# Optimization experiments

Hardware: AMD Instinct MI355X
Metric: run time of the kernel (lower is better)

The kernel has to match this reference:

```python
import jax, jax.numpy as jnp
import numpy as np

BN_EPS = 1e-5
L2_EPS = 1e-12  # F.normalize eps
K = 9           # kernel_size (dilation=1 so effective k = 9)
GROUPS = 4      # hard-coded groups in MRConv2d


def setup_inputs() -> dict:
    key = jax.random.key(0)
    k1, k2, k3 = jax.random.split(key, 3)
    B, C, H, W = 32, 192, 28, 28
    Cout = 384
    x = jax.random.normal(k1, (B, C, H, W), jnp.float32)
    # Conv2d(2C, Cout, 1, groups=4) weight is [Cout, 2C//4, 1, 1]; store as [Cout, 2C//4]
    fan_in = 2 * C // GROUPS
    conv_w = jax.random.normal(k2, (Cout, fan_in), jnp.float32) * np.sqrt(2.0 / fan_in)
    conv_b = jax.random.normal(k3, (Cout,), jnp.float32) * 0.05
    gamma = jnp.ones((Cout,), jnp.float32)
    beta = jnp.zeros((Cout,), jnp.float32)
    return {"x": x, "conv_w": conv_w, "conv_b": conv_b, "gamma": gamma, "beta": beta}


def _knn_idx(xf, k):
    """xf: (B, C, N) -> nn_idx: (B, N, k) via L2-normalized pairwise distance + topk."""
    xn = xf / jnp.maximum(jnp.linalg.norm(xf, axis=1, keepdims=True), L2_EPS)
    xt = xn.transpose(0, 2, 1)                       # (B, N, C)
    sq = jnp.sum(xt * xt, axis=-1, keepdims=True)    # (B, N, 1)
    inner = jnp.einsum('bnc,bmc->bnm', xt, xt)       # (B, N, N)
    dist = sq - 2.0 * inner + sq.transpose(0, 2, 1)
    _, nn_idx = jax.lax.top_k(-dist, k)              # (B, N, k)
    return nn_idx


def _forward(x, conv_w, conv_b, gamma, beta):
    B, C, H, W = x.shape
    N = H * W
    xf = x.reshape(B, C, N)
    # KNN graph built on detached features (torch: no_grad + x.detach for y when r=1)
    y = jax.lax.stop_gradient(xf)
    nn_idx = _knn_idx(y, K)                                            # (B, N, K)
    # gather neighbor features: xj[b,c,n,kk] = y[b,c,nn_idx[b,n,kk]]
    xj = jax.vmap(lambda yb, ib: yb[:, ib])(y, nn_idx)                 # (B, C, N, K)
    # max-relative: max_k (x_j - x_i); center gather of edge_index[1] is just xf
    rel = jnp.max(xj - xf[:, :, :, None], axis=-1)                     # (B, C, N)
    # cat([x.unsqueeze(2), rel.unsqueeze(2)], dim=2).reshape(B, 2C, N): channel-interleaved
    h = jnp.stack([xf, rel], axis=2).reshape(B, 2 * C, N)
    # grouped 1x1 conv, groups=4
    Cin = 2 * C
    Cout = conv_w.shape[0]
    hg = h.reshape(B, GROUPS, Cin // GROUPS, N)
    wg = conv_w.reshape(GROUPS, Cout // GROUPS, Cin // GROUPS)
    out = jnp.einsum('bgin,goi->bgon', hg, wg).reshape(B, Cout, N)
    out = out + conv_b[None, :, None]
    # BatchNorm2d (training-mode batch stats, biased variance)
    mean = jnp.mean(out, axis=(0, 2), keepdims=True)
    var = jnp.var(out, axis=(0, 2), keepdims=True)
    out = (out - mean) * jax.lax.rsqrt(var + BN_EPS)
    out = out * gamma[None, :, None] + beta[None, :, None]
    # exact (erf-based) GELU, matching torch.nn.GELU default
    out = jax.nn.gelu(out, approximate=False)
    return out.reshape(B, Cout, H, W)


def reference(x, conv_w, conv_b, gamma, beta):
    return _forward(x, conv_w, conv_b, gamma, beta)
```

## Files before the change

kernel.cpp:

```cpp
#include <hip/hip_runtime.h>

#define B_    32
#define C_    192
#define N_    784
#define NP_   1024
#define K_    9
#define COUT_ 384
#define NPTS_ (B_ * N_)
#define NTILES_ 224
#define DKW_  836

typedef __attribute__((ext_vector_type(8))) short short8;
typedef __attribute__((ext_vector_type(4))) float f32x4;

__device__ __forceinline__ unsigned int ford(float f) {
  unsigned int u = __float_as_uint(f);
  return u ^ ((u & 0x80000000u) ? 0xFFFFFFFFu : 0x80000000u);
}
__device__ __forceinline__ unsigned short f2bf(float f) {
  unsigned int u = __float_as_uint(f);
  u += 0x7FFFu + ((u >> 16) & 1u);
  return (unsigned short)(u >> 16);
}
__device__ __forceinline__ float bf2f(unsigned short h) {
  return __uint_as_float(((unsigned int)h) << 16);
}

__global__ __launch_bounds__(256) void norm_kernel(
    const float* __restrict__ x, short8* __restrict__ fragH,
    short8* __restrict__ fragL, float* __restrict__ sqp) {
  int t = threadIdx.x;
  int pl = t & 63, cg = t >> 6;
  int p = blockIdx.x * 64 + pl;
  int b = p / N_, n = p % N_;
  const float* xb = x + (size_t)b * C_ * N_ + n;

  __shared__ float red[4][64];
  __shared__ float nrmS[64];

  float part = 0.f;
  #pragma unroll 8
  for (int j = 0; j < 48; j++) {
    float v = xb[(size_t)(cg * 48 + j) * N_];
    part = __fmaf_rn(v, v, part);
  }
  red[cg][pl] = part;
  __syncthreads();
  if (t < 64) {
    float ssq = __fadd_rn(__fadd_rn(red[0][t], red[1][t]),
                          __fadd_rn(red[2][t], red[3][t]));
    nrmS[t] = fmaxf(__fsqrt_rn(ssq), 1e-12f);
  }
  __syncthreads();
  float nrm = nrmS[pl];
  int g = n >> 4, li = n & 15;
  float p2 = 0.f;
  #pragma unroll
  for (int s = 0; s < 6; s++) {
    int kslot = cg * 6 + s;
    int ks = kslot >> 2, kq = kslot & 3;
    union { short8 v; unsigned short u[8]; } ph, plo;
    #pragma unroll
    for (int j = 0; j < 8; j++) {
      float a = __fdiv_rn(xb[(size_t)(kslot * 8 + j) * N_], nrm);
      unsigned short h = f2bf(a);
      ph.u[j]  = h;
      plo.u[j] = f2bf(__fsub_rn(a, bf2f(h)));
      p2 = __fmaf_rn(a, a, p2);
    }
    size_t idx = (((size_t)b * 6 + ks) * 64 + g) * 64 + (kq * 16 + li);
    fragH[idx] = ph.v;
    fragL[idx] = plo.v;
  }
  red[cg][pl] = p2;
  __syncthreads();
  if (t < 64) {
    float sq = __fadd_rn(__fadd_rn(red[0][t], red[1][t]),
                         __fadd_rn(red[2][t], red[3][t]));
    int pp = blockIdx.x * 64 + t;
    sqp[(size_t)(pp / N_) * NP_ + (pp % N_)] = sq;
  }
}

__global__ __launch_bounds__(256) void knn_kernel(
    const short8* __restrict__ fragH, const short8* __restrict__ fragL,
    const float* __restrict__ sqp, int* __restrict__ nn9) {
  int wg = blockIdx.x;
  int r = wg & 7, j = wg >> 3;
  int b  = r + 8 * (j / 49);
  int qt = j % 49;
  int q0 = qt * 16;
  int t = threadIdx.x, lane = t & 63, w = t >> 6;

  __shared__ unsigned int dkS[16][DKW_];
  __shared__ float qsqS[16];

  for (int i = t; i < 16 * 52; i += 256)
    dkS[i / 52][784 + i % 52] = 0xFFFFFFFFu;
  if (t < 16) qsqS[t] = sqp[(size_t)b * NP_ + q0 + t];
  __syncthreads();

  const float* sqb = sqp + (size_t)b * NP_;
  const short8* fH = fragH + (size_t)b * 6 * 64 * 64;
  const short8* fL = fragL + (size_t)b * 6 * 64 * 64;

  short8 aH[6], aL[6];
  #pragma unroll
  for (int ks = 0; ks < 6; ks++) {
    aH[ks] = fH[((size_t)ks * 64 + qt) * 64 + lane];
    aL[ks] = fL[((size_t)ks * 64 + qt) * 64 + lane];
  }

  int colL = lane & 15, rq = lane >> 4;
  const int wstart = (w == 0) ? 0 : (w == 1) ? 13 : (w == 2) ? 26 : 39;
  const int wend   = (w == 0) ? 13 : (w == 1) ? 26 : (w == 2) ? 39 : 49;

  int g = wstart;
  for (; g + 1 < wend; g += 2) {
    int g0 = g, g1 = g + 1;
    short8 B0h[6], B0l[6], B1h[6], B1l[6];
    #pragma unroll
    for (int ks = 0; ks < 6; ks++) {
      B0h[ks] = fH[((size_t)ks * 64 + g0) * 64 + lane];
      B0l[ks] = fL[((size_t)ks * 64 + g0) * 64 + lane];
      B1h[ks] = fH[((size_t)ks * 64 + g1) * 64 + lane];
      B1l[ks] = fL[((size_t)ks * 64 + g1) * 64 + lane];
    }
    float cs0 = sqb[g0 * 16 + colL];
    float cs1 = sqb[g1 * 16 + colL];
    f32x4 a00 = {0.f, 0.f, 0.f, 0.f}, a01 = a00, a02 = a00;
    f32x4 a10 = a00, a11 = a00, a12 = a00;
    #pragma unroll
    for (int ks = 0; ks < 6; ks++) {
      a00 = __builtin_amdgcn_mfma_f32_16x16x32_bf16(aH[ks], B0h[ks], a00, 0, 0, 0);
      a01 = __builtin_amdgcn_mfma_f32_16x16x32_bf16(aH[ks], B0l[ks], a01, 0, 0, 0);
      a02 = __builtin_amdgcn_mfma_f32_16x16x32_bf16(aL[ks], B0h[ks], a02, 0, 0, 0);
      a10 = __builtin_amdgcn_mfma_f32_16x16x32_bf16(aH[ks], B1h[ks], a10, 0, 0, 0);
      a11 = __builtin_amdgcn_mfma_f32_16x16x32_bf16(aH[ks], B1l[ks], a11, 0, 0, 0);
      a12 = __builtin_amdgcn_mfma_f32_16x16x32_bf16(aL[ks], B1h[ks], a12, 0, 0, 0);
    }
    #pragma unroll
    for (int rr = 0; rr < 4; rr++) {
      int row = rq * 4 + rr;
      float qs = qsqS[row];
      float g0v = __fadd_rn(__fadd_rn(a00[rr], a01[rr]), a02[rr]);
      float g1v = __fadd_rn(__fadd_rn(a10[rr], a11[rr]), a12[rr]);
      float d0 = __fadd_rn(__fsub_rn(qs, __fmul_rn(2.0f, g0v)), cs0);
      float d1 = __fadd_rn(__fsub_rn(qs, __fmul_rn(2.0f, g1v)), cs1);
      dkS[row][g0 * 16 + colL] = ford(d0);
      dkS[row][g1 * 16 + colL] = ford(d1);
    }
  }
  if (g < wend) {
    int g0 = g;
    short8 B0h[6], B0l[6];
    #pragma unroll
    for (int ks = 0; ks < 6; ks++) {
      B0h[ks] = fH[((size_t)ks * 64 + g0) * 64 + lane];
      B0l[ks] = fL[((size_t)ks * 64 + g0) * 64 + lane];
    }
    float cs0 = sqb[g0 * 16 + colL];
    f32x4 a00 = {0.f, 0.f, 0.f, 0.f}, a01 = a00, a02 = a00;
    #pragma unroll
    for (int ks = 0; ks < 6; ks++) {
      a00 = __builtin_amdgcn_mfma_f32_16x16x32_bf16(aH[ks], B0h[ks], a00, 0, 0, 0);
      a01 = __builtin_amdgcn_mfma_f32_16x16x32_bf16(aH[ks], B0l[ks], a01, 0, 0, 0);
      a02 = __builtin_amdgcn_mfma_f32_16x16x32_bf16(aL[ks], B0h[ks], a02, 0, 0, 0);
    }
    #pragma unroll
    for (int rr = 0; rr < 4; rr++) {
      int row = rq * 4 + rr;
      float qs = qsqS[row];
      float g0v = __fadd_rn(__fadd_rn(a00[rr], a01[rr]), a02[rr]);
      float d0 = __fadd_rn(__fsub_rn(qs, __fmul_rn(2.0f, g0v)), cs0);
      dkS[row][g0 * 16 + colL] = ford(d0);
    }
  }
  __syncthreads();

  for (int s = 0; s < 4; s++) {
    int row = w * 4 + s;
    unsigned int bv = 0xFFFFFFFFu; int bi = lane;
    #pragma unroll
    for (int it = 0; it < 13; it++) {
      unsigned int k = dkS[row][lane + 64 * it];
      if (k < bv) { bv = k; bi = lane + 64 * it; }
    }
    int* o = nn9 + ((size_t)b * N_ + q0 + row) * K_;
    for (int kk = 0; kk < K_; kk++) {
      unsigned long long mk = ((unsigned long long)bv << 10) | (unsigned int)bi;
      #pragma unroll
      for (int off = 1; off < 64; off <<= 1) {
        unsigned long long v2 = __shfl_xor(mk, off);
        mk = v2 < mk ? v2 : mk;
      }
      int widx = (int)(mk & 1023u);
      if (lane == 0) o[kk] = widx;
      if ((widx & 63) == lane) {
        dkS[row][widx] = 0xFFFFFFFFu;
        bv = 0xFFFFFFFFu; bi = lane;
        #pragma unroll
        for (int it = 0; it < 13; it++) {
          unsigned int k = dkS[row][lane + 64 * it];
          if (k < bv) { bv = k; bi = lane + 64 * it; }
        }
      }
    }
  }
}

__global__ __launch_bounds__(256) void fconv_kernel(
    const float* __restrict__ x, const int* __restrict__ nn9,
    const float* __restrict__ w, const float* __restrict__ bias,
    float* __restrict__ outpre, float* __restrict__ psum,
    float* __restrict__ pss) {
  int nt = blockIdx.x;
  int g  = blockIdx.y;
  int b  = blockIdx.z;
  int n0 = nt * 112;
  int t = threadIdx.x;

  __shared__ float Wl[48][97];
  __shared__ float Hl[96][112];
  __shared__ unsigned short Il[112][K_];

  const int* isrc = nn9 + ((size_t)b * N_ + n0) * K_;
  for (int i = t; i < 112 * K_; i += 256)
    Il[i / K_][i % K_] = (unsigned short)isrc[i];
  const float* wsrc0 = w + (size_t)(g * 96) * 96;
  for (int i = t; i < 48 * 96; i += 256) Wl[i / 96][i % 96] = wsrc0[i];
  __syncthreads();

  const float* xb = x + (size_t)b * C_ * N_;
  for (int pos = t; pos < 48 * 112; pos += 256) {
    int cl = pos / 112, nl = pos % 112;
    const float* row = xb + (size_t)(g * 48 + cl) * N_;
    float xv = row[n0 + nl];
    float mx = -1e30f;
    #pragma unroll
    for (int k = 0; k < K_; k++) mx = fmaxf(mx, row[Il[nl][k]]);
    Hl[2 * cl][nl]     = xv;
    Hl[2 * cl + 1][nl] = mx - xv;
  }
  __syncthreads();

  int tx = t & 15, ty = t >> 4;
  int tidx = b * 7 + nt;

  for (int half = 0; half < 2; half++) {
    float o[3][7];
    #pragma unroll
    for (int i = 0; i < 3; i++)
      #pragma unroll
      for (int j = 0; j < 7; j++) o[i][j] = 0.f;

    for (int k = 0; k < 96; k++) {
      float w0 = Wl[ty * 3 + 0][k];
      float w1 = Wl[ty * 3 + 1][k];
      float w2 = Wl[ty * 3 + 2][k];
      #pragma unroll
      for (int j = 0; j < 7; j++) {
        float hv = Hl[k][tx * 7 + j];
        o[0][j] = __fmaf_rn(w0, hv, o[0][j]);
        o[1][j] = __fmaf_rn(w1, hv, o[1][j]);
        o[2][j] = __fmaf_rn(w2, hv, o[2][j]);
      }
    }

    #pragma unroll
    for (int i = 0; i < 3; i++) {
      int co = g * 96 + half * 48 + ty * 3 + i;
      float bv = bias[co];
      float s = 0.f, s2 = 0.f;
      float* orow = outpre + ((size_t)b * COUT_ + co) * N_ + n0 + tx * 7;
      #pragma unroll
      for (int j = 0; j < 7; j++) {
        float v = o[i][j] + bv;
        orow[j] = v;
        s += v; s2 += v * v;
      }
      #pragma unroll
      for (int off = 1; off < 16; off <<= 1) {
        s  += __shfl_xor(s, off);
        s2 += __shfl_xor(s2, off);
      }
      if (tx == 0) {
        psum[co * NTILES_ + tidx] = s;
        pss [co * NTILES_ + tidx] = s2;
      }
    }

    if (half == 0) {
      __syncthreads();
      const float* wsrc1 = w + (size_t)(g * 96 + 48) * 96;
      for (int i = t; i < 48 * 96; i += 256) Wl[i / 96][i % 96] = wsrc1[i];
      __syncthreads();
    }
  }
}

__global__ __launch_bounds__(64) void stats_kernel(
    const float* __restrict__ psum, const float* __restrict__ pss,
    const float* __restrict__ gamma, const float* __restrict__ beta,
    float* __restrict__ af, float* __restrict__ bf) {
  int co = blockIdx.x;
  int l = threadIdx.x;
  double s = 0.0, s2 = 0.0;
  for (int i = l; i < NTILES_; i += 64) {
    s  += (double)psum[co * NTILES_ + i];
    s2 += (double)pss [co * NTILES_ + i];
  }
  #pragma unroll
  for (int o = 32; o > 0; o >>= 1) { s += __shfl_xor(s, o); s2 += __shfl_xor(s2, o); }
  if (l == 0) {
    const double cnt = (double)NPTS_;
    double mean = s / cnt;
    double var  = s2 / cnt - mean * mean;
    double rstd = 1.0 / sqrt(var + 1e-5);
    double a = (double)gamma[co] * rstd;
    af[co] = (float)a;
    bf[co] = (float)((double)beta[co] - mean * a);
  }
}

__global__ __launch_bounds__(256) void act_kernel(
    const float* __restrict__ outpre, const float* __restrict__ af,
    const float* __restrict__ bf, float* __restrict__ out) {
  size_t i = ((size_t)blockIdx.x * 256 + threadIdx.x) * 4;
  int co = (int)((i / N_) % COUT_);
  float a = af[co], c = bf[co];
  float4 v = *(const float4*)(outpre + i);
  float y0 = a * v.x + c, y1 = a * v.y + c, y2 = a * v.z + c, y3 = a * v.w + c;
  const float is2 = 0.70710678118654752f;
  float4 r;
  r.x = 0.5f * y0 * (1.0f + erff(y0 * is2));
  r.y = 0.5f * y1 * (1.0f + erff(y1 * is2));
  r.z = 0.5f * y2 * (1.0f + erff(y2 * is2));
  r.w = 0.5f * y3 * (1.0f + erff(y3 * is2));
  *reinterpret_cast<float4*>(out + i) = r;
}

extern "C" void kernel_launch(void* const* d_in, const int* in_sizes, int n_in,
                              void* d_out, int out_size, void* d_ws, size_t ws_size,
                              hipStream_t stream) {
  const float* x      = (const float*)d_in[0];
  const float* conv_w = (const float*)d_in[1];
  const float* conv_b = (const float*)d_in[2];
  const float* gamma  = (const float*)d_in[3];
  const float* beta   = (const float*)d_in[4];
  float* out = (float*)d_out;

  float* buf0 = (float*)d_ws;
  short8* fragH = (short8*)buf0;
  short8* fragL = (short8*)(buf0 + 3145728);
  float*  sqp   = buf0 + 6291456;
  int*    nn9   = (int*)(buf0 + 6324224);
  float*  outpre = buf0 + 6550016;
  float*  psum  = buf0 + 16183808;
  float*  pss   = psum + COUT_ * NTILES_;
  float*  af    = pss + COUT_ * NTILES_;
  float*  bfv   = af + COUT_;

  hipLaunchKernelGGL(norm_kernel, dim3(NPTS_ / 64), dim3(256), 0, stream,
                     x, fragH, fragL, sqp);
  hipLaunchKernelGGL(knn_kernel, dim3(49 * B_), dim3(256), 0, stream,
                     fragH, fragL, sqp, nn9);
  hipLaunchKernelGGL(fconv_kernel, dim3(7, 4, B_), dim3(256), 0, stream,
                     x, nn9, conv_w, conv_b, outpre, psum, pss);
  hipLaunchKernelGGL(stats_kernel, dim3(COUT_), dim3(64), 0, stream,
                     psum, pss, gamma, beta, af, bfv);
  hipLaunchKernelGGL(act_kernel, dim3((B_ * COUT_ * N_) / (256 * 4)), dim3(256), 0, stream,
                     outpre, af, bfv, out);
}
```

Before: 210.0 us.

## Write point-major transposed copy of x and gather neighbors with vector loads

The norm kernel now also writes a point-major (B,N,C) copy of x into workspace, and the fused conv kernel gathers each neighbor's channel slice with contiguous float4 loads instead of strided scalar loads along channel rows. This turns the scattered per-channel gathers into coalesced row reads. The workspace is reordered so outpre overlaps the fragment buffers, which are dead by then. The cost is an extra full write of x in norm_kernel, and the per-thread stores into xT are strided by C, so they may coalesce poorly. Only 224 of 256 threads do the gather.

```diff
diff --git a/kernel.cpp b/kernel.cpp
--- a/kernel.cpp
+++ b/kernel.cpp
@@ -28,20 +28,23 @@
 
 __global__ __launch_bounds__(256) void norm_kernel(
     const float* __restrict__ x, short8* __restrict__ fragH,
-    short8* __restrict__ fragL, float* __restrict__ sqp) {
+    short8* __restrict__ fragL, float* __restrict__ sqp,
+    float* __restrict__ xT) {
   int t = threadIdx.x;
   int pl = t & 63, cg = t >> 6;
   int p = blockIdx.x * 64 + pl;
   int b = p / N_, n = p % N_;
   const float* xb = x + (size_t)b * C_ * N_ + n;
+  float* xTp = xT + (size_t)p * C_ + cg * 48;
 
   __shared__ float red[4][64];
   __shared__ float nrmS[64];
 
   float part = 0.f;
-  #pragma unroll 8
+  #pragma unroll
   for (int j = 0; j < 48; j++) {
     float v = xb[(size_t)(cg * 48 + j) * N_];
+    xTp[j] = v;
     part = __fmaf_rn(v, v, part);
   }
   red[cg][pl] = part;
@@ -210,7 +213,7 @@
 }
 
 __global__ __launch_bounds__(256) void fconv_kernel(
-    const float* __restrict__ x, const int* __restrict__ nn9,
+    const float* __restrict__ xT, const int* __restrict__ nn9,
     const float* __restrict__ w, const float* __restrict__ bias,
     float* __restrict__ outpre, float* __restrict__ psum,
     float* __restrict__ pss) {
@@ -231,16 +234,35 @@
   for (int i = t; i < 48 * 96; i += 256) Wl[i / 96][i % 96] = wsrc0[i];
   __syncthreads();
 
-  const float* xb = x + (size_t)b * C_ * N_;
-  for (int pos = t; pos < 48 * 112; pos += 256) {
-    int cl = pos / 112, nl = pos % 112;
-    const float* row = xb + (size_t)(g * 48 + cl) * N_;
-    float xv = row[n0 + nl];
-    float mx = -1e30f;
-    #pragma unroll
-    for (int k = 0; k < K_; k++) mx = fmaxf(mx, row[Il[nl][k]]);
-    Hl[2 * cl][nl]     = xv;
-    Hl[2 * cl + 1][nl] = mx - xv;
+  if (t < 224) {
+    int nl = t >> 1, half = t & 1;
+    const float* xrow = xT + ((size_t)b * N_ + n0 + nl) * C_ + g * 48 + half * 24;
+    float xv[24], mx[24];
+    #pragma unroll
+    for (int j = 0; j < 24; j += 4) {
+      float4 v = *(const float4*)(xrow + j);
+      xv[j] = v.x; xv[j + 1] = v.y; xv[j + 2] = v.z; xv[j + 3] = v.w;
+      mx[j] = -1e30f; mx[j + 1] = -1e30f; mx[j + 2] = -1e30f; mx[j + 3] = -1e30f;
+    }
+    #pragma unroll
+    for (int k = 0; k < K_; k++) {
+      int idx = Il[nl][k];
+      const float* nrow = xT + ((size_t)b * N_ + idx) * C_ + g * 48 + half * 24;
+      #pragma unroll
+      for (int j = 0; j < 24; j += 4) {
+        float4 v = *(const float4*)(nrow + j);
+        mx[j]     = fmaxf(mx[j], v.x);
+        mx[j + 1] = fmaxf(mx[j + 1], v.y);
+        mx[j + 2] = fmaxf(mx[j + 2], v.z);
+        mx[j + 3] = fmaxf(mx[j + 3], v.w);
+      }
+    }
+    #pragma unroll
+    for (int j = 0; j < 24; j++) {
+      int cl = half * 24 + j;
+      Hl[2 * cl][nl]     = xv[j];
+      Hl[2 * cl + 1][nl] = mx[j] - xv[j];
+    }
   }
   __syncthreads();
 
@@ -353,20 +375,21 @@
   float* buf0 = (float*)d_ws;
   short8* fragH = (short8*)buf0;
   short8* fragL = (short8*)(buf0 + 3145728);
-  float*  sqp   = buf0 + 6291456;
-  int*    nn9   = (int*)(buf0 + 6324224);
-  float*  outpre = buf0 + 6550016;
-  float*  psum  = buf0 + 16183808;
+  float*  outpre = buf0;
+  float*  sqp   = buf0 + 9633792;
+  int*    nn9   = (int*)(buf0 + 9666560);
+  float*  xT    = buf0 + 9892352;
+  float*  psum  = buf0 + 14709248;
   float*  pss   = psum + COUT_ * NTILES_;
   float*  af    = pss + COUT_ * NTILES_;
   float*  bfv   = af + COUT_;
 
   hipLaunchKernelGGL(norm_kernel, dim3(NPTS_ / 64), dim3(256), 0, stream,
-                     x, fragH, fragL, sqp);
+                     x, fragH, fragL, sqp, xT);
   hipLaunchKernelGGL(knn_kernel, dim3(49 * B_), dim3(256), 0, stream,
                      fragH, fragL, sqp, nn9);
   hipLaunchKernelGGL(fconv_kernel, dim3(7, 4, B_), dim3(256), 0, stream,
-                     x, nn9, conv_w, conv_b, outpre, psum, pss);
+                     xT, nn9, conv_w, conv_b, outpre, psum, pss);
   hipLaunchKernelGGL(stats_kernel, dim3(COUT_), dim3(64), 0, stream,
                      psum, pss, gamma, beta, af, bfv);
   hipLaunchKernelGGL(act_kernel, dim3((B_ * COUT_ * N_) / (256 * 4)), dim3(256), 0, stream,
```

Measured after the change: 200.5 us. -4.5%, faster.
